# Optimization experiments

Measured on AMD Instinct MI355X. Metric: run time of the kernel, lower is better.

The kernel has to match this reference:

```python
import jax, jax.numpy as jnp
import numpy as np

B, N, K = 8, 16384, 32
EPS = 1e-5


def setup_inputs() -> dict:
    key = jax.random.key(0)
    ks = jax.random.split(key, 11)
    xyz = jax.random.normal(ks[0], (B, N, 3), jnp.float32)
    intensity = jax.random.normal(ks[1], (B, 3, N), jnp.float32)
    indices = jax.random.randint(ks[2], (B, N, K), 0, N)
    # linear_p: Conv2d(3,3,1)+BN+ReLU, then Conv2d(3,1,1)
    w1 = jax.random.normal(ks[3], (3, 3), jnp.float32) * 0.3
    b1 = jax.random.normal(ks[4], (3,), jnp.float32) * 0.1
    gamma = jax.random.uniform(ks[5], (3,), jnp.float32, 0.5, 1.5)
    beta = jax.random.normal(ks[6], (3,), jnp.float32) * 0.1
    mean = jax.random.normal(ks[7], (3,), jnp.float32) * 0.1
    var = jax.random.uniform(ks[8], (3,), jnp.float32, 0.5, 1.5)
    w2 = jax.random.normal(ks[9], (1, 3), jnp.float32) * 0.3
    b2 = jax.random.normal(ks[10], (1,), jnp.float32) * 0.1
    return dict(xyz=xyz, intensity=intensity, indices=indices, w1=w1, b1=b1,
                gamma=gamma, beta=beta, mean=mean, var=var, w2=w2, b2=b2)


def reference(xyz, intensity, indices, w1, b1, gamma, beta, mean, var, w2, b2):
    # neighbor gathers (irregular access)
    xyz_nb = jax.vmap(lambda p, i: p[i])(xyz, indices)          # [B,N,K,3]
    i_nb = jax.vmap(lambda ft, i: ft[:, i])(intensity, indices)  # [B,3,N,K]
    # relative position + gaussian kernel
    pos = xyz_nb - xyz[:, :, None, :]                            # [B,N,K,3]
    pos_g = jnp.exp(-2.0 * pos * pos)
    pos_g = jnp.transpose(pos_g, (0, 3, 1, 2))                   # [B,3,N,K]
    # 1x1 conv (3->3) + eval-mode BN + ReLU
    h = jnp.einsum('oc,bcnk->bonk', w1, pos_g) + b1[None, :, None, None]
    scale = gamma / jnp.sqrt(var + EPS)
    h = (h - mean[None, :, None, None]) * scale[None, :, None, None] + beta[None, :, None, None]
    h = jax.nn.relu(h)
    # 1x1 conv (3->1), softmax over neighbors
    w = jnp.einsum('oc,bcnk->bonk', w2, h) + b2[None, :, None, None]  # [B,1,N,K]
    w = jax.nn.softmax(w, axis=-1)
    # weighted reduce over neighbors
    return jnp.sum(i_nb * w, axis=-1)                            # [B,3,N]
```

## Files before the change

kernel.cpp:

```cpp
#include <hip/hip_runtime.h>
#include <hip/hip_fp16.h>
#include <math.h>

#define PB 8
#define PN 16384
#define PK 32
#define PEPS 1e-5f
#define HALF_N 8192

__global__ __launch_bounds__(256) void sa_pack(
    const float* __restrict__ xyz,
    const float* __restrict__ intensity,
    uint4* __restrict__ packed,
    const float* __restrict__ w1, const float* __restrict__ b1,
    const float* __restrict__ gamma_, const float* __restrict__ beta_,
    const float* __restrict__ mean_, const float* __restrict__ var_,
    const float* __restrict__ w2, const float* __restrict__ b2,
    float* __restrict__ cst)
{
    const int t = blockIdx.x * 256 + threadIdx.x;
    const int b = t >> 14;
    const int n = t & (PN - 1);
    const float x = xyz[(long)t * 3 + 0];
    const float y = xyz[(long)t * 3 + 1];
    const float z = xyz[(long)t * 3 + 2];
    const float* ib = intensity + (long)b * 3 * PN;
    const float i0 = ib[0 * PN + n];
    const float i1 = ib[1 * PN + n];
    const float i2 = ib[2 * PN + n];

    union { __half2 h2[4]; uint4 u; } rec;
    rec.h2[0] = __halves2half2(__float2half_rn(x), __float2half_rn(y));
    rec.h2[1] = __halves2half2(__float2half_rn(z), __float2half_rn(0.f));
    rec.h2[2] = __halves2half2(__float2half_rn(i0), __float2half_rn(i1));
    rec.h2[3] = __halves2half2(__float2half_rn(i2), __float2half_rn(0.f));
    packed[t] = rec.u;

    if (t == 0) {
        for (int o = 0; o < 3; ++o) {
            const float sc = gamma_[o] * rsqrtf(var_[o] + PEPS);
            for (int c = 0; c < 3; ++c) cst[o * 3 + c] = w1[o * 3 + c] * sc;
            cst[9 + o]  = (b1[o] - mean_[o]) * sc + beta_[o];
            cst[12 + o] = w2[o];
        }
        cst[15] = b2[0];
    }
}

__global__ __launch_bounds__(512, 1) void sa_lds(
    const uint4* __restrict__ packed,
    const int*   __restrict__ indices,
    const float* __restrict__ cst,
    float* __restrict__ out)
{
    __shared__ uint2 sXYZ[HALF_N];
    __shared__ uint2 sINT[HALF_N];

    const int tid = threadIdx.x;
    const int q   = blockIdx.x * 512 + tid;
    const int b   = q >> 14;
    const int n   = q & (PN - 1);

    const float A00 = cst[0], A01 = cst[1], A02 = cst[2];
    const float A10 = cst[3], A11 = cst[4], A12 = cst[5];
    const float A20 = cst[6], A21 = cst[7], A22 = cst[8];
    const float d0 = cst[9], d1 = cst[10], d2 = cst[11];
    const float w0 = cst[12], w1v = cst[13], w2v = cst[14];
    const float bias2 = cst[15];

    const uint4 crec = packed[q];
    const float2 cxy = __half22float2(*(const __half2*)&crec.x);
    const float  cz  = __half2float(*(const __half*)&crec.y);

    int idxs[32];
    const int4* ip = (const int4*)(indices + (size_t)q * PK);
#pragma unroll
    for (int j = 0; j < 8; ++j) {
        const int4 v = ip[j];
        idxs[4 * j + 0] = v.x; idxs[4 * j + 1] = v.y;
        idxs[4 * j + 2] = v.z; idxs[4 * j + 3] = v.w;
    }

    const uint4* pb = packed + ((size_t)b << 14);

    float s = 0.f, a0 = 0.f, a1 = 0.f, a2 = 0.f;

    for (int h = 0; h < 2; ++h) {
        __syncthreads();
#pragma unroll
        for (int j = 0; j < 16; ++j) {
            const int r = tid + j * 512;
            const uint4 rec = pb[h * HALF_N + r];
            sXYZ[r] = make_uint2(rec.x, rec.y);
            sINT[r] = make_uint2(rec.z, rec.w);
        }
        __syncthreads();

#pragma unroll
        for (int k = 0; k < PK; ++k) {
            const int idx = idxs[k];
            if ((idx >> 13) == h) {
                const int local = idx & (HALF_N - 1);
                const uint2 xz = sXYZ[local];
                const uint2 it = sINT[local];

                const float2 nxy  = __half22float2(*(const __half2*)&xz.x);
                const float  nz   = __half2float(*(const __half*)&xz.y);
                const float2 ni01 = __half22float2(*(const __half2*)&it.x);
                const float  ni2  = __half2float(*(const __half*)&it.y);

                const float px = nxy.x - cxy.x;
                const float py = nxy.y - cxy.y;
                const float pz = nz - cz;

                const float g0 = __expf(-2.f * px * px);
                const float g1 = __expf(-2.f * py * py);
                const float g2 = __expf(-2.f * pz * pz);

                float h0 = fmaf(A00, g0, fmaf(A01, g1, fmaf(A02, g2, d0)));
                float h1 = fmaf(A10, g0, fmaf(A11, g1, fmaf(A12, g2, d1)));
                float h2 = fmaf(A20, g0, fmaf(A21, g1, fmaf(A22, g2, d2)));
                h0 = fmaxf(h0, 0.f); h1 = fmaxf(h1, 0.f); h2 = fmaxf(h2, 0.f);
                const float logit = fmaf(w0, h0, fmaf(w1v, h1, fmaf(w2v, h2, bias2)));

                const float e = __expf(logit);
                s += e;
                a0 = fmaf(e, ni01.x, a0);
                a1 = fmaf(e, ni01.y, a1);
                a2 = fmaf(e, ni2,    a2);
            }
        }
    }

    const float inv = 1.f / s;
    float* ob = out + (size_t)b * 3 * PN;
    ob[0 * PN + n] = a0 * inv;
    ob[1 * PN + n] = a1 * inv;
    ob[2 * PN + n] = a2 * inv;
}

__global__ __launch_bounds__(256) void sa_fallback(
    const float* __restrict__ xyz, const float* __restrict__ intensity,
    const int* __restrict__ indices,
    const float* __restrict__ w1, const float* __restrict__ b1,
    const float* __restrict__ gamma_, const float* __restrict__ beta_,
    const float* __restrict__ mean_, const float* __restrict__ var_,
    const float* __restrict__ w2, const float* __restrict__ b2,
    float* __restrict__ out)
{
    const int lane = threadIdx.x & 31;
    const int grp  = threadIdx.x >> 5;
    const long ng  = (long)blockIdx.x * 8 + grp;
    const int b = (int)(ng >> 14);
    const int n = (int)(ng & (PN - 1));

    float A[3][3], d[3], wv[3];
#pragma unroll
    for (int o = 0; o < 3; ++o) {
        const float sc = gamma_[o] * rsqrtf(var_[o] + PEPS);
#pragma unroll
        for (int c = 0; c < 3; ++c) A[o][c] = w1[o * 3 + c] * sc;
        d[o]  = (b1[o] - mean_[o]) * sc + beta_[o];
        wv[o] = w2[o];
    }
    const float bias2 = b2[0];
    const long bn = (long)b * PN + n;
    const float cx = xyz[bn * 3 + 0], cy = xyz[bn * 3 + 1], cz = xyz[bn * 3 + 2];
    const int idx = indices[bn * PK + lane];
    const long bi = (long)b * PN + idx;
    const float px = xyz[bi * 3 + 0] - cx;
    const float py = xyz[bi * 3 + 1] - cy;
    const float pz = xyz[bi * 3 + 2] - cz;
    const float g0 = __expf(-2.f * px * px);
    const float g1 = __expf(-2.f * py * py);
    const float g2 = __expf(-2.f * pz * pz);
    float logit = bias2;
#pragma unroll
    for (int o = 0; o < 3; ++o) {
        float h = A[o][0] * g0 + A[o][1] * g1 + A[o][2] * g2 + d[o];
        h = fmaxf(h, 0.f);
        logit = fmaf(wv[o], h, logit);
    }
    float m = logit;
#pragma unroll
    for (int s = 16; s > 0; s >>= 1) m = fmaxf(m, __shfl_xor(m, s, 64));
    const float e = __expf(logit - m);
    const float* ib = intensity + (long)b * 3 * PN;
    float ssum = e;
    float a0 = e * ib[0 * PN + idx];
    float a1 = e * ib[1 * PN + idx];
    float a2 = e * ib[2 * PN + idx];
#pragma unroll
    for (int s = 16; s > 0; s >>= 1) {
        ssum += __shfl_xor(ssum, s, 64);
        a0 += __shfl_xor(a0, s, 64);
        a1 += __shfl_xor(a1, s, 64);
        a2 += __shfl_xor(a2, s, 64);
    }
    if (lane == 0) {
        const float inv = 1.f / ssum;
        float* ob = out + (long)b * 3 * PN;
        ob[0 * PN + n] = a0 * inv;
        ob[1 * PN + n] = a1 * inv;
        ob[2 * PN + n] = a2 * inv;
    }
}

extern "C" void kernel_launch(void* const* d_in, const int* in_sizes, int n_in,
                              void* d_out, int out_size, void* d_ws, size_t ws_size,
                              hipStream_t stream) {
    const float* xyz       = (const float*)d_in[0];
    const float* intensity = (const float*)d_in[1];
    const int*   indices   = (const int*)d_in[2];
    const float* w1        = (const float*)d_in[3];
    const float* b1        = (const float*)d_in[4];
    const float* gamma_    = (const float*)d_in[5];
    const float* beta_     = (const float*)d_in[6];
    const float* mean_     = (const float*)d_in[7];
    const float* var_      = (const float*)d_in[8];
    const float* w2        = (const float*)d_in[9];
    const float* b2        = (const float*)d_in[10];
    float* out = (float*)d_out;

    const int points = PB * PN;
    const size_t rec_bytes = (size_t)points * 16;
    const size_t need = rec_bytes + 64;

    if (ws_size >= need) {
        uint4* packed = (uint4*)d_ws;
        float* cst = (float*)((char*)d_ws + rec_bytes);
        sa_pack<<<points / 256, 256, 0, stream>>>(xyz, intensity, packed,
                                                  w1, b1, gamma_, beta_, mean_,
                                                  var_, w2, b2, cst);
        sa_lds<<<points / 512, 512, 0, stream>>>(packed, indices, cst, out);
    } else {
        sa_fallback<<<points / 8, 256, 0, stream>>>(xyz, intensity, indices, w1, b1,
                                                    gamma_, beta_, mean_, var_, w2, b2, out);
    }
}
```

Before: 107.1 us.

## Split packed records into xyz and intensity arrays and stage each in LDS by phase

The pack kernel now writes separate half-precision xyz and intensity arrays instead of one interleaved record. The main kernel loads the whole batch's xyz (all 16384 points) into 128KB of LDS, computes all 32 softmax weights per point unconditionally, then reloads the same LDS buffer with intensities and does the weighted reduction. This removes the two-half pass with predicated neighbor loops, so each neighbor is processed once without branch divergence. The cost is 32 stored exponentials per thread in registers and an extra barrier-separated LDS refill.

```diff
diff --git a/kernel.cpp b/kernel.cpp
--- a/kernel.cpp
+++ b/kernel.cpp
@@ -6,12 +6,12 @@
 #define PN 16384
 #define PK 32
 #define PEPS 1e-5f
-#define HALF_N 8192
 
 __global__ __launch_bounds__(256) void sa_pack(
     const float* __restrict__ xyz,
     const float* __restrict__ intensity,
-    uint4* __restrict__ packed,
+    uint2* __restrict__ pxyz,
+    uint2* __restrict__ pint,
     const float* __restrict__ w1, const float* __restrict__ b1,
     const float* __restrict__ gamma_, const float* __restrict__ beta_,
     const float* __restrict__ mean_, const float* __restrict__ var_,
@@ -29,12 +29,13 @@
     const float i1 = ib[1 * PN + n];
     const float i2 = ib[2 * PN + n];
 
-    union { __half2 h2[4]; uint4 u; } rec;
-    rec.h2[0] = __halves2half2(__float2half_rn(x), __float2half_rn(y));
-    rec.h2[1] = __halves2half2(__float2half_rn(z), __float2half_rn(0.f));
-    rec.h2[2] = __halves2half2(__float2half_rn(i0), __float2half_rn(i1));
-    rec.h2[3] = __halves2half2(__float2half_rn(i2), __float2half_rn(0.f));
-    packed[t] = rec.u;
+    union { __half2 h2[2]; uint2 u; } rx, ri;
+    rx.h2[0] = __halves2half2(__float2half_rn(x), __float2half_rn(y));
+    rx.h2[1] = __halves2half2(__float2half_rn(z), __float2half_rn(0.f));
+    ri.h2[0] = __halves2half2(__float2half_rn(i0), __float2half_rn(i1));
+    ri.h2[1] = __halves2half2(__float2half_rn(i2), __float2half_rn(0.f));
+    pxyz[t] = rx.u;
+    pint[t] = ri.u;
 
     if (t == 0) {
         for (int o = 0; o < 3; ++o) {
@@ -47,14 +48,14 @@
     }
 }
 
-__global__ __launch_bounds__(512, 1) void sa_lds(
-    const uint4* __restrict__ packed,
+__global__ __launch_bounds__(512, 1) void sa_lds2(
+    const uint2* __restrict__ pxyz,
+    const uint2* __restrict__ pint,
     const int*   __restrict__ indices,
     const float* __restrict__ cst,
     float* __restrict__ out)
 {
-    __shared__ uint2 sXYZ[HALF_N];
-    __shared__ uint2 sINT[HALF_N];
+    __shared__ uint4 sbuf[PN / 2];
 
     const int tid = threadIdx.x;
     const int q   = blockIdx.x * 512 + tid;
@@ -68,7 +69,7 @@
     const float w0 = cst[12], w1v = cst[13], w2v = cst[14];
     const float bias2 = cst[15];
 
-    const uint4 crec = packed[q];
+    const uint2 crec = pxyz[q];
     const float2 cxy = __half22float2(*(const __half2*)&crec.x);
     const float  cz  = __half2float(*(const __half*)&crec.y);
 
@@ -81,55 +82,66 @@
         idxs[4 * j + 2] = v.z; idxs[4 * j + 3] = v.w;
     }
 
-    const uint4* pb = packed + ((size_t)b << 14);
-
-    float s = 0.f, a0 = 0.f, a1 = 0.f, a2 = 0.f;
-
-    for (int h = 0; h < 2; ++h) {
-        __syncthreads();
+    const uint2* sx = (const uint2*)sbuf;
+
+    {
+        const uint4* src = (const uint4*)(pxyz + ((size_t)b << 14));
 #pragma unroll
         for (int j = 0; j < 16; ++j) {
             const int r = tid + j * 512;
-            const uint4 rec = pb[h * HALF_N + r];
-            sXYZ[r] = make_uint2(rec.x, rec.y);
-            sINT[r] = make_uint2(rec.z, rec.w);
+            sbuf[r] = src[r];
         }
-        __syncthreads();
-
-#pragma unroll
-        for (int k = 0; k < PK; ++k) {
-            const int idx = idxs[k];
-            if ((idx >> 13) == h) {
-                const int local = idx & (HALF_N - 1);
-                const uint2 xz = sXYZ[local];
-                const uint2 it = sINT[local];
-
-                const float2 nxy  = __half22float2(*(const __half2*)&xz.x);
-                const float  nz   = __half2float(*(const __half*)&xz.y);
-                const float2 ni01 = __half22float2(*(const __half2*)&it.x);
-                const float  ni2  = __half2float(*(const __half*)&it.y);
-
-                const float px = nxy.x - cxy.x;
-                const float py = nxy.y - cxy.y;
-                const float pz = nz - cz;
-
-                const float g0 = __expf(-2.f * px * px);
-                const float g1 = __expf(-2.f * py * py);
-                const float g2 = __expf(-2.f * pz * pz);
-
-                float h0 = fmaf(A00, g0, fmaf(A01, g1, fmaf(A02, g2, d0)));
-                float h1 = fmaf(A10, g0, fmaf(A11, g1, fmaf(A12, g2, d1)));
-                float h2 = fmaf(A20, g0, fmaf(A21, g1, fmaf(A22, g2, d2)));
-                h0 = fmaxf(h0, 0.f); h1 = fmaxf(h1, 0.f); h2 = fmaxf(h2, 0.f);
-                const float logit = fmaf(w0, h0, fmaf(w1v, h1, fmaf(w2v, h2, bias2)));
-
-                const float e = __expf(logit);
-                s += e;
-                a0 = fmaf(e, ni01.x, a0);
-                a1 = fmaf(e, ni01.y, a1);
-                a2 = fmaf(e, ni2,    a2);
-            }
+    }
+    __syncthreads();
+
+    float ev[32];
+    float s = 0.f;
+#pragma unroll
+    for (int k = 0; k < PK; ++k) {
+        const uint2 xz = sx[idxs[k]];
+        const float2 nxy = __half22float2(*(const __half2*)&xz.x);
+        const float  nz  = __half2float(*(const __half*)&xz.y);
+
+        const float px = nxy.x - cxy.x;
+        const float py = nxy.y - cxy.y;
+        const float pz = nz - cz;
+
+        const float g0 = __expf(-2.f * px * px);
+        const float g1 = __expf(-2.f * py * py);
+        const float g2 = __expf(-2.f * pz * pz);
+
+        float h0 = fmaf(A00, g0, fmaf(A01, g1, fmaf(A02, g2, d0)));
+        float h1 = fmaf(A10, g0, fmaf(A11, g1, fmaf(A12, g2, d1)));
+        float h2 = fmaf(A20, g0, fmaf(A21, g1, fmaf(A22, g2, d2)));
+        h0 = fmaxf(h0, 0.f); h1 = fmaxf(h1, 0.f); h2 = fmaxf(h2, 0.f);
+        const float logit = fmaf(w0, h0, fmaf(w1v, h1, fmaf(w2v, h2, bias2)));
+
+        const float e = __expf(logit);
+        ev[k] = e;
+        s += e;
+    }
+
+    __syncthreads();
+    {
+        const uint4* src = (const uint4*)(pint + ((size_t)b << 14));
+#pragma unroll
+        for (int j = 0; j < 16; ++j) {
+            const int r = tid + j * 512;
+            sbuf[r] = src[r];
         }
+    }
+    __syncthreads();
+
+    float a0 = 0.f, a1 = 0.f, a2 = 0.f;
+#pragma unroll
+    for (int k = 0; k < PK; ++k) {
+        const uint2 it = sx[idxs[k]];
+        const float2 i01 = __half22float2(*(const __half2*)&it.x);
+        const float  i2  = __half2float(*(const __half*)&it.y);
+        const float e = ev[k];
+        a0 = fmaf(e, i01.x, a0);
+        a1 = fmaf(e, i01.y, a1);
+        a2 = fmaf(e, i2,    a2);
     }
 
     const float inv = 1.f / s;
@@ -223,16 +235,17 @@
     float* out = (float*)d_out;
 
     const int points = PB * PN;
-    const size_t rec_bytes = (size_t)points * 16;
-    const size_t need = rec_bytes + 64;
+    const size_t arr_bytes = (size_t)points * 8;
+    const size_t need = 2 * arr_bytes + 64;
 
     if (ws_size >= need) {
-        uint4* packed = (uint4*)d_ws;
-        float* cst = (float*)((char*)d_ws + rec_bytes);
-        sa_pack<<<points / 256, 256, 0, stream>>>(xyz, intensity, packed,
+        uint2* pxyz = (uint2*)d_ws;
+        uint2* pint = (uint2*)((char*)d_ws + arr_bytes);
+        float* cst  = (float*)((char*)d_ws + 2 * arr_bytes);
+        sa_pack<<<points / 256, 256, 0, stream>>>(xyz, intensity, pxyz, pint,
                                                   w1, b1, gamma_, beta_, mean_,
                                                   var_, w2, b2, cst);
-        sa_lds<<<points / 512, 512, 0, stream>>>(packed, indices, cst, out);
+        sa_lds2<<<points / 512, 512, 0, stream>>>(pxyz, pint, indices, cst, out);
     } else {
         sa_fallback<<<points / 8, 256, 0, stream>>>(xyz, intensity, indices, w1, b1,
                                                     gamma_, beta_, mean_, var_, w2, b2, out);
```

Result: faster. 101.9 us (-4.8%).
